# Kernel optimization log

Measured on AMD Instinct MI355X. Metric: run time of the kernel, lower is better.

Reference implementation:

```python
import jax, jax.numpy as jnp
import numpy as np

EMBED_DIM, HIDDEN_DIM, NUM_BINS = 1280, 256, 10

def setup_inputs() -> dict:
    key = jax.random.key(0)
    ks = jax.random.split(key, 7)
    s_in = 1.0 / np.sqrt(EMBED_DIM)
    s_h = 1.0 / np.sqrt(HIDDEN_DIM)
    return {
        "x": jax.random.normal(ks[0], (2, 384, EMBED_DIM), dtype=jnp.float32),
        "Wi": jax.random.uniform(ks[1], (EMBED_DIM, HIDDEN_DIM), jnp.float32, -s_in, s_in),
        "bi": jax.random.uniform(ks[2], (HIDDEN_DIM,), jnp.float32, -s_in, s_in),
        "Wj": jax.random.uniform(ks[3], (EMBED_DIM, HIDDEN_DIM), jnp.float32, -s_in, s_in),
        "bj": jax.random.uniform(ks[4], (HIDDEN_DIM,), jnp.float32, -s_in, s_in),
        "Wo": jax.random.uniform(ks[5], (HIDDEN_DIM, NUM_BINS), jnp.float32, -s_h, s_h),
        "bo": jax.random.uniform(ks[6], (NUM_BINS,), jnp.float32, -s_h, s_h),
    }

def reference(x, Wi, bi, Wj, bj, Wo, bo):
    # x: [B, L, D]
    xi = x @ Wi + bi              # [B, L, H]
    xj = x @ Wj + bj              # [B, L, H]
    pair = xi[:, :, None, :] * xj[:, None, :, :]   # [B, L, L, H]
    h = jax.nn.relu(pair)
    return h @ Wo + bo            # [B, L, L, num_bins]
```

## Files before the change

### kernel.cpp

```cpp
#include <hip/hip_runtime.h>

#define LSEQ 384
#define EMBED 1280
#define HID 256
#define NBINS 10
#define GM 768
#define KP 512

typedef __attribute__((ext_vector_type(8))) short short8;
typedef __attribute__((ext_vector_type(4))) short short4v;
typedef __attribute__((ext_vector_type(4))) float float4v;
typedef __attribute__((ext_vector_type(2))) float float2v;

__device__ __forceinline__ unsigned bfbits(float f) {
    unsigned u = __builtin_bit_cast(unsigned, f);
    return (u + 0x7fffu + ((u >> 16) & 1u)) >> 16;
}
__device__ __forceinline__ short f2bf(float f) { return (short)bfbits(f); }

__device__ __forceinline__ void load16_to_lds(const void* g, void* l) {
    __builtin_amdgcn_global_load_lds(
        (const __attribute__((address_space(1))) unsigned int*)g,
        (__attribute__((address_space(3))) unsigned int*)l, 16, 0, 0);
}

__global__ __launch_bounds__(256) void k_prep(
    const float* __restrict__ x, const float* __restrict__ Wi, const float* __restrict__ Wj,
    short* __restrict__ xb, short* __restrict__ WT)
{
    __shared__ float tile[32][33];
    const int t = threadIdx.x;
    int bx = blockIdx.x;
    if (bx < 480) {
        const int idx = bx * 256 + t;
        const float4v a = ((const float4v*)x)[idx * 2];
        const float4v b = ((const float4v*)x)[idx * 2 + 1];
        short8 o;
        o[0] = f2bf(a.x); o[1] = f2bf(a.y); o[2] = f2bf(a.z); o[3] = f2bf(a.w);
        o[4] = f2bf(b.x); o[5] = f2bf(b.y); o[6] = f2bf(b.z); o[7] = f2bf(b.w);
        ((short8*)xb)[idx] = o;
    } else {
        bx -= 480;
        const int isJ = bx >= 320 ? 1 : 0;
        if (isJ) bx -= 320;
        const int tk = bx % 40, tn = bx / 40;
        const int k0 = tk * 32, n0 = tn * 32;
        const float* __restrict__ W = isJ ? Wj : Wi;
        const int r = t >> 3, c4 = (t & 7) * 4;
        const float4v v = *(const float4v*)(W + (size_t)(k0 + r) * HID + n0 + c4);
        tile[r][c4 + 0] = v.x; tile[r][c4 + 1] = v.y;
        tile[r][c4 + 2] = v.z; tile[r][c4 + 3] = v.w;
        __syncthreads();
        const int n = r, kc = c4;
        short4v o;
        o.x = f2bf(tile[kc + 0][n]); o.y = f2bf(tile[kc + 1][n]);
        o.z = f2bf(tile[kc + 2][n]); o.w = f2bf(tile[kc + 3][n]);
        *(short4v*)(WT + (size_t)(isJ * HID + n0 + n) * EMBED + k0 + kc) = o;
    }
}

__global__ __launch_bounds__(256) void k_gemm(
    const short* __restrict__ xb, const short* __restrict__ WT, float* __restrict__ C)
{
    __shared__ short As[2][32 * 64];
    __shared__ short Bs[2][32 * 64];
    const int tid = threadIdx.x;
    const int lane = tid & 63, w = tid >> 6;
    const int mh = w & 1, nh = w >> 1;
    const int l15 = lane & 15, q = lane >> 4;
    const int m0 = blockIdx.x * 32, n0 = blockIdx.y * 32;
    const int lrow = lane >> 3, lcol = (lane & 7) * 8;

    const short* agp = xb + (size_t)(m0 + 8 * w + lrow) * EMBED + lcol;
    const short* bgp = WT + (size_t)(n0 + 8 * w + lrow) * EMBED + lcol;

    float4v acc = {0.f, 0.f, 0.f, 0.f};

    load16_to_lds(agp, &As[0][w * 512]);
    load16_to_lds(bgp, &Bs[0][w * 512]);
    __syncthreads();

    for (int ks = 0; ks < 20; ++ks) {
        const int cur = ks & 1;
        if (ks < 19) {
            load16_to_lds(agp + (ks + 1) * 64, &As[1 - cur][w * 512]);
            load16_to_lds(bgp + (ks + 1) * 64, &Bs[1 - cur][w * 512]);
        }
#pragma unroll
        for (int kk = 0; kk < 2; ++kk) {
            const short8 af = *(const short8*)&As[cur][(mh * 16 + l15) * 64 + kk * 32 + q * 8];
            const short8 bf = *(const short8*)&Bs[cur][(nh * 16 + l15) * 64 + kk * 32 + q * 8];
            acc = __builtin_amdgcn_mfma_f32_16x16x32_bf16(af, bf, acc, 0, 0, 0);
        }
        __syncthreads();
    }

#pragma unroll
    for (int r = 0; r < 4; ++r)
        C[(size_t)(m0 + mh * 16 + q * 4 + r) * KP + n0 + nh * 16 + l15] = acc[r];
}

__global__ __launch_bounds__(256) void k_pack(
    const float* __restrict__ C, const float* __restrict__ Wo,
    const float* __restrict__ bi, const float* __restrict__ bj,
    short* __restrict__ Aef, short* __restrict__ Bef)
{
    __shared__ float xrow[HID];
    __shared__ float woL[NBINS * HID];
    const int t = threadIdx.x, m = blockIdx.x;

    xrow[t] = C[(size_t)m * KP + t] + bi[t];
#pragma unroll
    for (int c = 0; c < NBINS; ++c) woL[c * HID + t] = Wo[(size_t)t * NBINS + c];

    const float vj = C[(size_t)m * KP + HID + t] + bj[t];
    Bef[(size_t)m * KP + t]       = f2bf(fmaxf(vj, 0.f));
    Bef[(size_t)m * KP + HID + t] = f2bf(fmaxf(-vj, 0.f));
    __syncthreads();

    const int k = 2 * t;
    const int h = k & (HID - 1);
    float v0, v1;
    if (t < 128) { v0 = fmaxf(xrow[h], 0.f);  v1 = fmaxf(xrow[h + 1], 0.f); }
    else         { v0 = fmaxf(-xrow[h], 0.f); v1 = fmaxf(-xrow[h + 1], 0.f); }

#pragma unroll
    for (int n = 0; n < NBINS; ++n) {
        const unsigned lo = bfbits(v0 * woL[n * HID + h]);
        const unsigned hi = bfbits(v1 * woL[n * HID + h + 1]);
        ((unsigned*)(Aef + ((size_t)n * GM + m) * KP))[t] = (hi << 16) | lo;
    }
}

__global__ __launch_bounds__(256) void k2_pair(
    const short* __restrict__ Aef, const short* __restrict__ Bef,
    const float* __restrict__ bo, float* __restrict__ out)
{
    __shared__ __align__(16) char smem[45056];
    short* As = (short*)smem;
    short* Bs = (short*)(smem + 40960);
    float* sout = (float*)smem;

    const int tid = threadIdx.x;
    const int lane = tid & 63, w = tid >> 6;
    const int ih = w & 1, nb = (w >> 1) * 5;
    const int l15 = lane & 15, q = lane >> 4;
    const int b = blockIdx.z;
    const int i0 = blockIdx.x * 32, j0 = blockIdx.y * 32;

    const size_t arow0 = (size_t)(b * LSEQ + i0);
    const size_t brow0 = (size_t)(b * LSEQ + j0);
    const int srow = lane >> 2;
    const int skb = (lane & 3) * 8;

    float4v acc[2][5];
#pragma unroll
    for (int jh = 0; jh < 2; ++jh)
#pragma unroll
        for (int nn = 0; nn < 5; ++nn) acc[jh][nn] = (float4v){0.f, 0.f, 0.f, 0.f};

#define STAGE_K2(ks, buf)                                                               \
    {                                                                                   \
        const int k0_ = (ks) * 32;                                                      \
        short* AsB = As + (buf) * 10240;                                                \
        short* BsB = Bs + (buf) * 1024;                                                 \
        const int p1 = w, p2 = w + 4;                                                   \
        _Pragma("unroll")                                                               \
        for (int hh = 0; hh < 2; ++hh) {                                                \
            load16_to_lds(Aef + ((size_t)p1 * GM + arow0 + hh * 16 + srow) * KP + k0_ + skb, \
                          AsB + p1 * 1024 + hh * 512);                                  \
            load16_to_lds(Aef + ((size_t)p2 * GM + arow0 + hh * 16 + srow) * KP + k0_ + skb, \
                          AsB + p2 * 1024 + hh * 512);                                  \
        }                                                                               \
        if (w < 2) {                                                                    \
            const int p3 = 8 + w;                                                       \
            _Pragma("unroll")                                                           \
            for (int hh = 0; hh < 2; ++hh)                                              \
                load16_to_lds(Aef + ((size_t)p3 * GM + arow0 + hh * 16 + srow) * KP + k0_ + skb, \
                              AsB + p3 * 1024 + hh * 512);                              \
        } else {                                                                        \
            load16_to_lds(Bef + (brow0 + (w - 2) * 16 + srow) * KP + k0_ + skb,         \
                          BsB + (w - 2) * 512);                                         \
        }                                                                               \
    }

    STAGE_K2(0, 0)
    __syncthreads();

    for (int ks = 0; ks < 16; ++ks) {
        const int cur = ks & 1;
        if (ks < 15) STAGE_K2(ks + 1, 1 - cur)
        const short* AsB = As + cur * 10240;
        const short* BsB = Bs + cur * 1024;
        const short8 bfr0 = *(const short8*)(BsB + (0 * 16 + l15) * 32 + q * 8);
        const short8 bfr1 = *(const short8*)(BsB + (1 * 16 + l15) * 32 + q * 8);
#pragma unroll
        for (int nn = 0; nn < 5; ++nn) {
            const short8 afr = *(const short8*)(AsB + (nb + nn) * 1024 + (ih * 16 + l15) * 32 + q * 8);
            acc[0][nn] = __builtin_amdgcn_mfma_f32_16x16x32_bf16(afr, bfr0, acc[0][nn], 0, 0, 0);
            acc[1][nn] = __builtin_amdgcn_mfma_f32_16x16x32_bf16(afr, bfr1, acc[1][nn], 0, 0, 0);
        }
        __syncthreads();
    }

    float bov[NBINS];
    const float2v* bop = (const float2v*)bo;
#pragma unroll
    for (int c = 0; c < 5; ++c) { float2v tv = bop[c]; bov[2 * c] = tv.x; bov[2 * c + 1] = tv.y; }

#pragma unroll
    for (int jh = 0; jh < 2; ++jh)
#pragma unroll
        for (int nn = 0; nn < 5; ++nn)
#pragma unroll
            for (int r = 0; r < 4; ++r)
                sout[((ih * 16 + q * 4 + r) * 32 + (jh * 16 + l15)) * NBINS + nb + nn] =
                    acc[jh][nn][r] + bov[nb + nn];
    __syncthreads();

    const float2v* s2 = (const float2v*)sout;
#pragma unroll
    for (int t = 0; t < 20; ++t) {
        const int f = t * 256 + tid;
        const int row = f / 160;
        const int rq = f - row * 160;
        float2v* dst = (float2v*)(out + ((size_t)(b * LSEQ + i0 + row) * LSEQ + j0) * NBINS);
        dst[rq] = s2[f];
    }
}

extern "C" void kernel_launch(void* const* d_in, const int* in_sizes, int n_in,
                              void* d_out, int out_size, void* d_ws, size_t ws_size,
                              hipStream_t stream)
{
    const float* x  = (const float*)d_in[0];
    const float* Wi = (const float*)d_in[1];
    const float* bi = (const float*)d_in[2];
    const float* Wj = (const float*)d_in[3];
    const float* bj = (const float*)d_in[4];
    const float* Wo = (const float*)d_in[5];
    const float* bo = (const float*)d_in[6];
    float* out = (float*)d_out;

    char* p = (char*)d_ws;
    float* C   = (float*)p;                 p += (size_t)GM * KP * 4;
    short* xb  = (short*)p;                 p += (size_t)GM * EMBED * 2;
    short* WT  = (short*)p;                 p += (size_t)KP * EMBED * 2;
    short* Aef = (short*)p;                 p += (size_t)NBINS * GM * KP * 2;
    short* Bef = (short*)p;

    k_prep<<<1120, 256, 0, stream>>>(x, Wi, Wj, xb, WT);
    k_gemm<<<dim3(GM / 32, KP / 32), 256, 0, stream>>>(xb, WT, C);
    k_pack<<<GM, 256, 0, stream>>>(C, Wo, bi, bj, Aef, Bef);
    k2_pair<<<dim3(LSEQ / 32, LSEQ / 32, 2), 256, 0, stream>>>(Aef, Bef, bo, out);
}
```

Before: 107.5 us.

## Fuse projection GEMM with pack stage and load MFMA fragments directly from global

Merges the projection GEMM and the pack kernel into one kernel. The bias, relu split and Wo scaling now run in the GEMM epilogue through a small LDS tile, which removes the fp32 C intermediate and one launch. Both the GEMM and the pair kernel drop their LDS double-buffered global_load_lds staging and read MFMA fragments straight from global memory, relying on L2/L1 for reuse. This cuts LDS use and barriers, but risks more redundant global traffic and exposed load latency.

```diff
diff --git a/kernel.cpp b/kernel.cpp
--- a/kernel.cpp
+++ b/kernel.cpp
@@ -17,12 +17,6 @@
     return (u + 0x7fffu + ((u >> 16) & 1u)) >> 16;
 }
 __device__ __forceinline__ short f2bf(float f) { return (short)bfbits(f); }
-
-__device__ __forceinline__ void load16_to_lds(const void* g, void* l) {
-    __builtin_amdgcn_global_load_lds(
-        (const __attribute__((address_space(1))) unsigned int*)g,
-        (__attribute__((address_space(3))) unsigned int*)l, 16, 0, 0);
-}
 
 __global__ __launch_bounds__(256) void k_prep(
     const float* __restrict__ x, const float* __restrict__ Wi, const float* __restrict__ Wj,
@@ -59,76 +53,88 @@
     }
 }
 
-__global__ __launch_bounds__(256) void k_gemm(
-    const short* __restrict__ xb, const short* __restrict__ WT, float* __restrict__ C)
-{
-    __shared__ short As[2][32 * 64];
-    __shared__ short Bs[2][32 * 64];
+__global__ __launch_bounds__(256) void k_gemm_pack(
+    const short* __restrict__ xb, const short* __restrict__ WT,
+    const float* __restrict__ bi, const float* __restrict__ bj, const float* __restrict__ Wo,
+    short* __restrict__ Aef, short* __restrict__ Bef)
+{
+    __shared__ float sC[32 * 32];
+    __shared__ float woS[32 * NBINS];
+
     const int tid = threadIdx.x;
     const int lane = tid & 63, w = tid >> 6;
     const int mh = w & 1, nh = w >> 1;
     const int l15 = lane & 15, q = lane >> 4;
     const int m0 = blockIdx.x * 32, n0 = blockIdx.y * 32;
-    const int lrow = lane >> 3, lcol = (lane & 7) * 8;
-
-    const short* agp = xb + (size_t)(m0 + 8 * w + lrow) * EMBED + lcol;
-    const short* bgp = WT + (size_t)(n0 + 8 * w + lrow) * EMBED + lcol;
+    const bool isI = (n0 < HID);
+
+    if (isI) {
+        for (int t = tid; t < 32 * NBINS; t += 256) woS[t] = Wo[n0 * NBINS + t];
+    }
+
+    const short* ap = xb + (size_t)(m0 + mh * 16 + l15) * EMBED + q * 8;
+    const short* bp = WT + (size_t)(n0 + nh * 16 + l15) * EMBED + q * 8;
 
     float4v acc = {0.f, 0.f, 0.f, 0.f};
-
-    load16_to_lds(agp, &As[0][w * 512]);
-    load16_to_lds(bgp, &Bs[0][w * 512]);
+#pragma unroll 8
+    for (int ks = 0; ks < EMBED / 32; ++ks) {
+        const short8 af = *(const short8*)(ap + ks * 32);
+        const short8 bf = *(const short8*)(bp + ks * 32);
+        acc = __builtin_amdgcn_mfma_f32_16x16x32_bf16(af, bf, acc, 0, 0, 0);
+    }
+
+    const int ncol = n0 + nh * 16 + l15;
+    const float bv = isI ? bi[ncol] : bj[ncol - HID];
+#pragma unroll
+    for (int r = 0; r < 4; ++r)
+        sC[(mh * 16 + q * 4 + r) * 32 + nh * 16 + l15] = acc[r] + bv;
     __syncthreads();
 
-    for (int ks = 0; ks < 20; ++ks) {
-        const int cur = ks & 1;
-        if (ks < 19) {
-            load16_to_lds(agp + (ks + 1) * 64, &As[1 - cur][w * 512]);
-            load16_to_lds(bgp + (ks + 1) * 64, &Bs[1 - cur][w * 512]);
+    const int mr = tid >> 3;
+    const int m = m0 + mr;
+    const int hq = (tid & 7) * 4;
+    float v[4];
+#pragma unroll
+    for (int c = 0; c < 4; ++c) v[c] = sC[mr * 32 + hq + c];
+
+    if (isI) {
+        const int hbase = n0 + hq;
+#pragma unroll
+        for (int nb = 0; nb < NBINS; ++nb) {
+            float wv[4];
+#pragma unroll
+            for (int c = 0; c < 4; ++c) wv[c] = woS[(hq + c) * NBINS + nb];
+            unsigned dp[2], dm[2];
+#pragma unroll
+            for (int g = 0; g < 2; ++g) {
+                const unsigned p0 = bfbits(fmaxf(v[2 * g], 0.f) * wv[2 * g]);
+                const unsigned p1 = bfbits(fmaxf(v[2 * g + 1], 0.f) * wv[2 * g + 1]);
+                const unsigned m0_ = bfbits(fmaxf(-v[2 * g], 0.f) * wv[2 * g]);
+                const unsigned m1_ = bfbits(fmaxf(-v[2 * g + 1], 0.f) * wv[2 * g + 1]);
+                dp[g] = (p1 << 16) | p0;
+                dm[g] = (m1_ << 16) | m0_;
+            }
+            unsigned* basep = (unsigned*)(Aef + ((size_t)nb * GM + m) * KP + hbase);
+            unsigned* basem = (unsigned*)(Aef + ((size_t)nb * GM + m) * KP + HID + hbase);
+            basep[0] = dp[0]; basep[1] = dp[1];
+            basem[0] = dm[0]; basem[1] = dm[1];
         }
-#pragma unroll
-        for (int kk = 0; kk < 2; ++kk) {
-            const short8 af = *(const short8*)&As[cur][(mh * 16 + l15) * 64 + kk * 32 + q * 8];
-            const short8 bf = *(const short8*)&Bs[cur][(nh * 16 + l15) * 64 + kk * 32 + q * 8];
-            acc = __builtin_amdgcn_mfma_f32_16x16x32_bf16(af, bf, acc, 0, 0, 0);
+    } else {
+        const int hbase = (n0 - HID) + hq;
+        unsigned dp[2], dm[2];
+#pragma unroll
+        for (int g = 0; g < 2; ++g) {
+            const unsigned p0 = bfbits(fmaxf(v[2 * g], 0.f));
+            const unsigned p1 = bfbits(fmaxf(v[2 * g + 1], 0.f));
+            const unsigned m0_ = bfbits(fmaxf(-v[2 * g], 0.f));
+            const unsigned m1_ = bfbits(fmaxf(-v[2 * g + 1], 0.f));
+            dp[g] = (p1 << 16) | p0;
+            dm[g] = (m1_ << 16) | m0_;
         }
-        __syncthreads();
-    }
-
-#pragma unroll
-    for (int r = 0; r < 4; ++r)
-        C[(size_t)(m0 + mh * 16 + q * 4 + r) * KP + n0 + nh * 16 + l15] = acc[r];
-}
-
-__global__ __launch_bounds__(256) void k_pack(
-    const float* __restrict__ C, const float* __restrict__ Wo,
-    const float* __restrict__ bi, const float* __restrict__ bj,
-    short* __restrict__ Aef, short* __restrict__ Bef)
-{
-    __shared__ float xrow[HID];
-    __shared__ float woL[NBINS * HID];
-    const int t = threadIdx.x, m = blockIdx.x;
-
-    xrow[t] = C[(size_t)m * KP + t] + bi[t];
-#pragma unroll
-    for (int c = 0; c < NBINS; ++c) woL[c * HID + t] = Wo[(size_t)t * NBINS + c];
-
-    const float vj = C[(size_t)m * KP + HID + t] + bj[t];
-    Bef[(size_t)m * KP + t]       = f2bf(fmaxf(vj, 0.f));
-    Bef[(size_t)m * KP + HID + t] = f2bf(fmaxf(-vj, 0.f));
-    __syncthreads();
-
-    const int k = 2 * t;
-    const int h = k & (HID - 1);
-    float v0, v1;
-    if (t < 128) { v0 = fmaxf(xrow[h], 0.f);  v1 = fmaxf(xrow[h + 1], 0.f); }
-    else         { v0 = fmaxf(-xrow[h], 0.f); v1 = fmaxf(-xrow[h + 1], 0.f); }
-
-#pragma unroll
-    for (int n = 0; n < NBINS; ++n) {
-        const unsigned lo = bfbits(v0 * woL[n * HID + h]);
-        const unsigned hi = bfbits(v1 * woL[n * HID + h + 1]);
-        ((unsigned*)(Aef + ((size_t)n * GM + m) * KP))[t] = (hi << 16) | lo;
+        unsigned* basep = (unsigned*)(Bef + (size_t)m * KP + hbase);
+        unsigned* basem = (unsigned*)(Bef + (size_t)m * KP + HID + hbase);
+        basep[0] = dp[0]; basep[1] = dp[1];
+        basem[0] = dm[0]; basem[1] = dm[1];
     }
 }
 
@@ -136,22 +142,17 @@
     const short* __restrict__ Aef, const short* __restrict__ Bef,
     const float* __restrict__ bo, float* __restrict__ out)
 {
-    __shared__ __align__(16) char smem[45056];
-    short* As = (short*)smem;
-    short* Bs = (short*)(smem + 40960);
-    float* sout = (float*)smem;
+    __shared__ float sout[32 * 32 * NBINS];
 
     const int tid = threadIdx.x;
     const int lane = tid & 63, w = tid >> 6;
-    const int ih = w & 1, nb = (w >> 1) * 5;
+    const int ih = w & 1, nb0 = (w >> 1) * 5;
     const int l15 = lane & 15, q = lane >> 4;
     const int b = blockIdx.z;
     const int i0 = blockIdx.x * 32, j0 = blockIdx.y * 32;
 
-    const size_t arow0 = (size_t)(b * LSEQ + i0);
-    const size_t brow0 = (size_t)(b * LSEQ + j0);
-    const int srow = lane >> 2;
-    const int skb = (lane & 3) * 8;
+    const short* aBase = Aef + ((size_t)nb0 * GM + (size_t)(b * LSEQ + i0 + ih * 16 + l15)) * KP + q * 8;
+    const short* bBase = Bef + (size_t)(b * LSEQ + j0 + l15) * KP + q * 8;
 
     float4v acc[2][5];
 #pragma unroll
@@ -159,48 +160,16 @@
 #pragma unroll
         for (int nn = 0; nn < 5; ++nn) acc[jh][nn] = (float4v){0.f, 0.f, 0.f, 0.f};
 
-#define STAGE_K2(ks, buf)                                                               \
-    {                                                                                   \
-        const int k0_ = (ks) * 32;                                                      \
-        short* AsB = As + (buf) * 10240;                                                \
-        short* BsB = Bs + (buf) * 1024;                                                 \
-        const int p1 = w, p2 = w + 4;                                                   \
-        _Pragma("unroll")                                                               \
-        for (int hh = 0; hh < 2; ++hh) {                                                \
-            load16_to_lds(Aef + ((size_t)p1 * GM + arow0 + hh * 16 + srow) * KP + k0_ + skb, \
-                          AsB + p1 * 1024 + hh * 512);                                  \
-            load16_to_lds(Aef + ((size_t)p2 * GM + arow0 + hh * 16 + srow) * KP + k0_ + skb, \
-                          AsB + p2 * 1024 + hh * 512);                                  \
-        }                                                                               \
-        if (w < 2) {                                                                    \
-            const int p3 = 8 + w;                                                       \
-            _Pragma("unroll")                                                           \
-            for (int hh = 0; hh < 2; ++hh)                                              \
-                load16_to_lds(Aef + ((size_t)p3 * GM + arow0 + hh * 16 + srow) * KP + k0_ + skb, \
-                              AsB + p3 * 1024 + hh * 512);                              \
-        } else {                                                                        \
-            load16_to_lds(Bef + (brow0 + (w - 2) * 16 + srow) * KP + k0_ + skb,         \
-                          BsB + (w - 2) * 512);                                         \
-        }                                                                               \
-    }
-
-    STAGE_K2(0, 0)
-    __syncthreads();
-
-    for (int ks = 0; ks < 16; ++ks) {
-        const int cur = ks & 1;
-        if (ks < 15) STAGE_K2(ks + 1, 1 - cur)
-        const short* AsB = As + cur * 10240;
-        const short* BsB = Bs + cur * 1024;
-        const short8 bfr0 = *(const short8*)(BsB + (0 * 16 + l15) * 32 + q * 8);
-        const short8 bfr1 = *(const short8*)(BsB + (1 * 16 + l15) * 32 + q * 8);
+#pragma unroll 2
+    for (int ks = 0; ks < KP / 32; ++ks) {
+        const short8 b0 = *(const short8*)(bBase + ks * 32);
+        const short8 b1 = *(const short8*)(bBase + (size_t)16 * KP + ks * 32);
 #pragma unroll
         for (int nn = 0; nn < 5; ++nn) {
-            const short8 afr = *(const short8*)(AsB + (nb + nn) * 1024 + (ih * 16 + l15) * 32 + q * 8);
-            acc[0][nn] = __builtin_amdgcn_mfma_f32_16x16x32_bf16(afr, bfr0, acc[0][nn], 0, 0, 0);
-            acc[1][nn] = __builtin_amdgcn_mfma_f32_16x16x32_bf16(afr, bfr1, acc[1][nn], 0, 0, 0);
+            const short8 af = *(const short8*)(aBase + (size_t)nn * GM * KP + ks * 32);
+            acc[0][nn] = __builtin_amdgcn_mfma_f32_16x16x32_bf16(af, b0, acc[0][nn], 0, 0, 0);
+            acc[1][nn] = __builtin_amdgcn_mfma_f32_16x16x32_bf16(af, b1, acc[1][nn], 0, 0, 0);
         }
-        __syncthreads();
     }
 
     float bov[NBINS];
@@ -214,8 +183,8 @@
         for (int nn = 0; nn < 5; ++nn)
 #pragma unroll
             for (int r = 0; r < 4; ++r)
-                sout[((ih * 16 + q * 4 + r) * 32 + (jh * 16 + l15)) * NBINS + nb + nn] =
-                    acc[jh][nn][r] + bov[nb + nn];
+                sout[((ih * 16 + q * 4 + r) * 32 + (jh * 16 + l15)) * NBINS + nb0 + nn] =
+                    acc[jh][nn][r] + bov[nb0 + nn];
     __syncthreads();
 
     const float2v* s2 = (const float2v*)sout;
@@ -243,14 +212,12 @@
     float* out = (float*)d_out;
 
     char* p = (char*)d_ws;
-    float* C   = (float*)p;                 p += (size_t)GM * KP * 4;
     short* xb  = (short*)p;                 p += (size_t)GM * EMBED * 2;
     short* WT  = (short*)p;                 p += (size_t)KP * EMBED * 2;
     short* Aef = (short*)p;                 p += (size_t)NBINS * GM * KP * 2;
     short* Bef = (short*)p;
 
     k_prep<<<1120, 256, 0, stream>>>(x, Wi, Wj, xb, WT);
-    k_gemm<<<dim3(GM / 32, KP / 32), 256, 0, stream>>>(xb, WT, C);
-    k_pack<<<GM, 256, 0, stream>>>(C, Wo, bi, bj, Aef, Bef);
+    k_gemm_pack<<<dim3(GM / 32, KP / 32), 256, 0, stream>>>(xb, WT, bi, bj, Wo, Aef, Bef);
     k2_pair<<<dim3(LSEQ / 32, LSEQ / 32, 2), 256, 0, stream>>>(Aef, Bef, bo, out);
 }
```

New measurement: 125.2 us. 16.4% more time.
